# Performance work log

Hardware: AMD Instinct MI355X
Metric: run time of the kernel (lower is better)

The kernel has to match this reference:

```python
import jax, jax.numpy as jnp
import numpy as np

EPS = 1e-8
SLOPE = 0.2  # default negative_slope in VNLinearLeakyReLU
N_KNN = 4
GS_EPS = 1e-6
NOISE_SCALE = 0.1


def vn_linear(x, W):
    # x: (B, Cin, 3, ...), W: (Cout, Cin) -> (B, Cout, 3, ...)
    return jnp.einsum('oc,bc...->bo...', W, x)


def vn_linear_leaky_relu(x, Wf, Wd):
    p = vn_linear(x, Wf)
    d = vn_linear(x, Wd)
    dot = jnp.sum(p * d, axis=2, keepdims=True)
    d2 = jnp.sum(d * d, axis=2, keepdims=True)
    neg = p - (dot / (d2 + EPS)) * d
    return SLOPE * p + (1.0 - SLOPE) * jnp.where(dot >= 0, p, neg)


def vn_max_pool(x, Wd):
    # pools over the last axis using a learned direction
    d = vn_linear(x, Wd)
    dot = jnp.sum(x * d, axis=2, keepdims=True)          # (B,C,1,...,N)
    idx = jnp.argmax(dot, axis=-1)                       # (B,C,1,...)
    idx = jnp.broadcast_to(idx, x.shape[:-1])[..., None]
    return jnp.take_along_axis(x, idx, axis=-1)[..., 0]


def get_graph_feature(x, knn):
    # x: (B, C, 3, N) -> (B, 2C, 3, N, knn)
    B, C, _, N = x.shape
    xf = x.reshape(B, 3 * C, N)
    xx = jnp.sum(xf * xf, axis=1)                        # (B,N)
    inner = jnp.einsum('bdn,bdm->bnm', xf, xf)           # (B,N,N)
    neg_dist = 2.0 * inner - xx[:, :, None] - xx[:, None, :]
    _, idx = jax.lax.top_k(neg_dist, knn)                # (B,N,knn)
    pts = x.transpose(0, 3, 1, 2)                        # (B,N,C,3)
    nbrs = pts[jnp.arange(B)[:, None, None], idx]        # (B,N,knn,C,3)
    ctr = jnp.broadcast_to(pts[:, :, None], nbrs.shape)
    feat = jnp.concatenate([nbrs - ctr, ctr], axis=3)    # (B,N,knn,2C,3)
    return feat.transpose(0, 3, 4, 1, 2)


def batched_gram_schmidt_3d(M):
    # orthonormalize the columns of (B,3,3)
    def nrm(v):
        return v / (jnp.linalg.norm(v, axis=-1, keepdims=True) + EPS)
    v1, v2, v3 = M[:, :, 0], M[:, :, 1], M[:, :, 2]
    e1 = nrm(v1)
    u2 = v2 - jnp.sum(e1 * v2, -1, keepdims=True) * e1
    e2 = nrm(u2)
    u3 = v3 - jnp.sum(e1 * v3, -1, keepdims=True) * e1 - jnp.sum(e2 * v3, -1, keepdims=True) * e2
    e3 = nrm(u3)
    return jnp.stack([e1, e2, e3], axis=-1)


def setup_inputs() -> dict:
    key = jax.random.key(0)
    ks = jax.random.split(key, 10)
    b, n, d_node, d_edge, kk, dim = 4, 2048, 2, 4, 4, 32  # dim = 96 // 3
    return {
        'node_features': jax.random.normal(ks[0], (b, n, 3, d_node), jnp.float32),
        'edge_features': jax.random.normal(ks[1], (b, n, n, d_edge), jnp.float32),
        'idx': jnp.arange(b, dtype=jnp.int32),
        'k': kk,
        'W1f': jax.random.normal(ks[2], (dim, 2 * d_node), jnp.float32) * 0.3,
        'W1d': jax.random.normal(ks[3], (dim, 2 * d_node), jnp.float32) * 0.3,
        'Wp1': jax.random.normal(ks[4], (dim, dim), jnp.float32) * 0.1,
        'Wp3': jax.random.normal(ks[5], (dim, dim), jnp.float32) * 0.1,
        'Wh2': jax.random.normal(ks[6], (3, dim), jnp.float32) * 0.1,
        'z': jax.random.normal(ks[7], (b, kk, n, 3, d_node), jnp.float32) * NOISE_SCALE,
        'gs_noise': jax.random.normal(ks[8], (b, kk, 3, 3), jnp.float32),
    }


def reference(node_features, edge_features, idx, k, W1f, W1d, Wp1, Wp3, Wh2, z, gs_noise):
    b, n, _, d = node_features.shape
    # replicate k times and add invariant noise (fixed_noise=False path)
    x = jnp.broadcast_to(node_features[:, None], (b, k, n, 3, d)) + z
    x = x.reshape(b * k, n, 3, d).transpose(0, 3, 2, 1)   # (bk, d, 3, n)
    g = get_graph_feature(x, N_KNN)                       # (bk, 2d, 3, n, knn)
    h = vn_linear_leaky_relu(g, W1f, W1d)                 # (bk, dim, 3, n, knn)
    x1 = vn_max_pool(h, Wp1)                              # (bk, dim, 3, n)
    pooled = vn_max_pool(x1, Wp3)                         # (bk, dim, 3)
    pk = vn_linear(pooled, Wh2)                           # (bk, 3, 3)
    pk = pk.transpose(0, 2, 1).reshape(b, k, 3, 3)
    pk = pk + GS_EPS * gs_noise
    R = batched_gram_schmidt_3d(pk.reshape(b * k, 3, 3))
    det = jnp.linalg.det(R)                               # SO3 sign fix on column 0
    R = R.at[:, :, 0].multiply(det[:, None])
    return R.reshape(b, k, 3, 3)
```

## Files before the change

### kernel.cpp

```cpp
#include <hip/hip_runtime.h>
#include <math.h>

#define EPSF    1e-8f
#define SLOPEF  0.2f
#define GS_EPSF 1e-6f

#define NB   4
#define KZ   4
#define BKT  16
#define NPT  2048
#define DIM  32

#define COMP(v,kk) ((kk)==0?(v).x:(kk)==1?(v).y:(kk)==2?(v).z:(v).w)

__device__ __forceinline__ void fma4(float4& acc, float s, const float4& v) {
  acc.x = fmaf(s, v.x, acc.x); acc.y = fmaf(s, v.y, acc.y);
  acc.z = fmaf(s, v.z, acc.z); acc.w = fmaf(s, v.w, acc.w);
}

__global__ __launch_bounds__(256) void prep_coords(
    const float* __restrict__ node, const float* __restrict__ z,
    const float* __restrict__ Wp1, const float* __restrict__ Wp3,
    float4* __restrict__ pts, float4* __restrict__ wpk) {
  if (blockIdx.x == 0) {
    int i = threadIdx.x;
    int og = i & 7, c = i >> 3;
    wpk[i]       = make_float4(Wp1[og * 32 + c], Wp1[(og + 8) * 32 + c],
                               Wp1[(og + 16) * 32 + c], Wp1[(og + 24) * 32 + c]);
    wpk[256 + i] = make_float4(Wp3[og * 32 + c], Wp3[(og + 8) * 32 + c],
                               Wp3[(og + 16) * 32 + c], Wp3[(og + 24) * 32 + c]);
  }
  int t = blockIdx.x * 256 + threadIdx.x;
  if (t >= BKT * NPT) return;
  int bk = t >> 11, n = t & (NPT - 1);
  int b = bk >> 2, kz = bk & 3;
  const float2* np2 = (const float2*)(node + (size_t)(b * NPT + n) * 6);
  const float2* zp2 = (const float2*)(z + (size_t)((b * KZ + kz) * NPT + n) * 6);
  float ch[6];
#pragma unroll
  for (int j = 0; j < 3; ++j) {
    float2 a = np2[j], c = zp2[j];
    ch[j]     = a.x + c.x;
    ch[3 + j] = a.y + c.y;
  }
  float xx = 0.f;
#pragma unroll
  for (int h = 0; h < 6; ++h) xx = fmaf(ch[h], ch[h], xx);
  pts[(size_t)t * 2 + 0] = make_float4(ch[0], ch[1], ch[2], ch[3]);
  pts[(size_t)t * 2 + 1] = make_float4(ch[4], ch[5], xx, 0.f);
}

__device__ __forceinline__ void ins3(float s, int j,
    float& v0, float& v1, float& v2, int& i0, int& i1, int& i2) {
  bool c2 = s > v2;
  float nv2 = c2 ? s : v2; int ni2 = c2 ? j : i2;
  bool c1 = nv2 > v1;
  float u1v = c1 ? nv2 : v1, u2v = c1 ? v1 : nv2;
  int   u1i = c1 ? ni2 : i1, u2i = c1 ? i1 : ni2;
  bool c0 = u1v > v0;
  v1 = c0 ? v0 : u1v; i1 = c0 ? i0 : u1i;
  v0 = c0 ? u1v : v0; i0 = c0 ? u1i : i0;
  v2 = u2v; i2 = u2i;
}

__device__ __forceinline__ void ce(float& vx, int& ix, float& vy, int& iy) {
  float av = vx, bv = vy; int ai = ix, bi = iy;
  bool sw = (bv > av) || (bv == av && bi < ai);
  vx = sw ? bv : av; vy = sw ? av : bv;
  ix = sw ? bi : ai; iy = sw ? ai : bi;
}

__device__ __forceinline__ float score7(const float4& qa, const float4& qb,
                                        const float4& A, const float4& B) {
  float s = qa.x * A.x;
  s = fmaf(qa.y, A.y, s);
  s = fmaf(qa.z, A.z, s);
  s = fmaf(qa.w, A.w, s);
  s = fmaf(qb.x, B.x, s);
  s = fmaf(qb.y, B.y, s);
  s = fmaf(-0.5f, B.z, s);
  return s;
}

template <bool SELF>
__device__ __forceinline__ void scan128(const float4* __restrict__ pp, int j0, int q,
    const float4 qa, const float4 qb,
    float& v0, float& v1, float& v2, int& i0, int& i1, int& i2) {
  for (int t = 0; t < 128; t += 4) {
    float4 A0 = pp[2 * t + 0], B0 = pp[2 * t + 1];
    float4 A1 = pp[2 * t + 2], B1 = pp[2 * t + 3];
    float4 A2 = pp[2 * t + 4], B2 = pp[2 * t + 5];
    float4 A3 = pp[2 * t + 6], B3 = pp[2 * t + 7];
    float s0 = score7(qa, qb, A0, B0);
    float s1 = score7(qa, qb, A1, B1);
    float s2 = score7(qa, qb, A2, B2);
    float s3 = score7(qa, qb, A3, B3);
    int jb = j0 + t;
    if (SELF) {
      if (jb + 0 == q) s0 = -INFINITY;
      if (jb + 1 == q) s1 = -INFINITY;
      if (jb + 2 == q) s2 = -INFINITY;
      if (jb + 3 == q) s3 = -INFINITY;
    }
    ins3(s0, jb + 0, v0, v1, v2, i0, i1, i2);
    ins3(s1, jb + 1, v0, v1, v2, i0, i1, i2);
    ins3(s2, jb + 2, v0, v1, v2, i0, i1, i2);
    ins3(s3, jb + 3, v0, v1, v2, i0, i1, i2);
  }
}

__global__ __launch_bounds__(1024) void knn_kernel(
    const float4* __restrict__ pts, int4* __restrict__ knn4) {
  __shared__ float4 lv[16][64];
  __shared__ int4   li[16][64];
  int lane = threadIdx.x & 63;
  int w = threadIdx.x >> 6;
  int bk = blockIdx.x >> 5, qg = blockIdx.x & 31;
  int base = bk * NPT;
  int q = qg * 64 + lane;
  float4 qa = pts[(size_t)(base + q) * 2 + 0];
  float4 qb = pts[(size_t)(base + q) * 2 + 1];
  int j0 = __builtin_amdgcn_readfirstlane(w * 128);
  const float4* pp = pts + ((size_t)base + j0) * 2;
  float v0 = -INFINITY, v1 = -INFINITY, v2 = -INFINITY;
  int   i0 = 0x7fffffff, i1 = 0x7fffffff, i2 = 0x7fffffff;
  if (w == (qg >> 1)) scan128<true >(pp, j0, q, qa, qb, v0, v1, v2, i0, i1, i2);
  else                scan128<false>(pp, j0, q, qa, qb, v0, v1, v2, i0, i1, i2);
  lv[w][lane] = make_float4(v0, v1, v2, -INFINITY);
  li[w][lane] = make_int4(i0, i1, i2, 0x7fffffff);
  __syncthreads();
#pragma unroll
  for (int str = 8; str >= 1; str >>= 1) {
    if (w < str) {
      float4 av = lv[w][lane];        int4 ai = li[w][lane];
      float4 bv = lv[w + str][lane];  int4 bi = li[w + str][lane];
      float a0 = av.x, a1 = av.y, a2 = av.z, a3 = av.w;
      int   c0 = ai.x, c1 = ai.y, c2 = ai.z, c3 = ai.w;
      float s4 = bv.w, s5 = bv.z, s6 = bv.y, s7 = bv.x;
      int   t4 = bi.w, t5 = bi.z, t6 = bi.y, t7 = bi.x;
      ce(a0, c0, s4, t4); ce(a1, c1, s5, t5);
      ce(a2, c2, s6, t6); ce(a3, c3, s7, t7);
      ce(a0, c0, a2, c2); ce(a1, c1, a3, c3);
      ce(a0, c0, a1, c1); ce(a2, c2, a3, c3);
      lv[w][lane] = make_float4(a0, a1, a2, a3);
      li[w][lane] = make_int4(c0, c1, c2, c3);
    }
    __syncthreads();
  }
  if (w == 0) {
    int4 r = li[0][lane];
    knn4[base + q] = make_int4(q, r.x, r.y, r.z);
  }
}

__global__ __launch_bounds__(128) void feature_kernel(
    const float4* __restrict__ pts, const int4* __restrict__ knn4,
    const float* __restrict__ W1f, const float* __restrict__ W1d,
    const float4* __restrict__ wpk,
    float4* __restrict__ partials) {
  __shared__ float4 hlds[16][97];
  __shared__ float  dlds[16][33];
  int p = threadIdx.x >> 3;
  int og = threadIdx.x & 7;
  int bk = blockIdx.x >> 7, pb = blockIdx.x & 127;
  int n = (pb << 4) | p;
  int base = bk * NPT;
  float4 ca = pts[(size_t)(base + n) * 2 + 0], cbv = pts[(size_t)(base + n) * 2 + 1];
  float ct[6] = {ca.x, ca.y, ca.z, ca.w, cbv.x, cbv.y};
  float w1f[4][4], w1d[4][4];
#pragma unroll
  for (int m = 0; m < 4; ++m) {
    float4 wf = reinterpret_cast<const float4*>(W1f)[og + 8 * m];
    float4 wd = reinterpret_cast<const float4*>(W1d)[og + 8 * m];
    w1f[m][0] = wf.x; w1f[m][1] = wf.y; w1f[m][2] = wf.z; w1f[m][3] = wf.w;
    w1d[m][0] = wd.x; w1d[m][1] = wd.y; w1d[m][2] = wd.z; w1d[m][3] = wd.w;
  }
  int4 nb = knn4[base + n];
  int nbi[4] = {nb.x, nb.y, nb.z, nb.w};
  float h[4][4][3];
#pragma unroll
  for (int kk = 0; kk < 4; ++kk) {
    int mi = nbi[kk];
    float4 A = pts[(size_t)(base + mi) * 2 + 0], B = pts[(size_t)(base + mi) * 2 + 1];
    float nc[6] = {A.x, A.y, A.z, A.w, B.x, B.y};
    float G[4][3];
#pragma unroll
    for (int j = 0; j < 3; ++j) {
      G[0][j] = nc[j] - ct[j];
      G[1][j] = nc[3 + j] - ct[3 + j];
      G[2][j] = ct[j];
      G[3][j] = ct[3 + j];
    }
#pragma unroll
    for (int m = 0; m < 4; ++m) {
      float pvv[3], dv[3];
#pragma unroll
      for (int j = 0; j < 3; ++j) {
        float a = 0.f, dd = 0.f;
#pragma unroll
        for (int c = 0; c < 4; ++c) { a = fmaf(w1f[m][c], G[c][j], a); dd = fmaf(w1d[m][c], G[c][j], dd); }
        pvv[j] = a; dv[j] = dd;
      }
      float dot = pvv[0] * dv[0] + pvv[1] * dv[1] + pvv[2] * dv[2];
      float d2  = dv[0] * dv[0] + dv[1] * dv[1] + dv[2] * dv[2];
      float fac = dot / (d2 + EPSF);
#pragma unroll
      for (int j = 0; j < 3; ++j) {
        float negj = pvv[j] - fac * dv[j];
        float sel = (dot >= 0.f) ? pvv[j] : negj;
        h[m][kk][j] = SLOPEF * pvv[j] + (1.f - SLOPEF) * sel;
      }
    }
  }
#pragma unroll
  for (int m = 0; m < 4; ++m)
#pragma unroll
    for (int j = 0; j < 3; ++j)
      hlds[p][(og + 8 * m) * 3 + j] =
          make_float4(h[m][0][j], h[m][1][j], h[m][2][j], h[m][3][j]);
  __syncthreads();
  float4 d1j0[4], d1j1[4], d1j2[4];
#pragma unroll
  for (int m = 0; m < 4; ++m) {
    d1j0[m] = make_float4(0.f, 0.f, 0.f, 0.f);
    d1j1[m] = make_float4(0.f, 0.f, 0.f, 0.f);
    d1j2[m] = make_float4(0.f, 0.f, 0.f, 0.f);
  }
  for (int c = 0; c < 32; ++c) {
    float4 wv = wpk[c * 8 + og];
    float4 h0 = hlds[p][c * 3 + 0];
    float4 h1 = hlds[p][c * 3 + 1];
    float4 h2 = hlds[p][c * 3 + 2];
#pragma unroll
    for (int m = 0; m < 4; ++m) {
      float wm = COMP(wv, m);
      fma4(d1j0[m], wm, h0);
      fma4(d1j1[m], wm, h1);
      fma4(d1j2[m], wm, h2);
    }
  }
  float x1[4][3];
#pragma unroll
  for (int m = 0; m < 4; ++m) {
    float best = -INFINITY;
    float xa = 0.f, xb = 0.f, xc = 0.f;
#pragma unroll
    for (int kk = 0; kk < 4; ++kk) {
      float dt = h[m][kk][0] * COMP(d1j0[m], kk)
               + h[m][kk][1] * COMP(d1j1[m], kk)
               + h[m][kk][2] * COMP(d1j2[m], kk);
      if (dt > best) { best = dt; xa = h[m][kk][0]; xb = h[m][kk][1]; xc = h[m][kk][2]; }
    }
    x1[m][0] = xa; x1[m][1] = xb; x1[m][2] = xc;
  }
  __syncthreads();
#pragma unroll
  for (int m = 0; m < 4; ++m)
    hlds[p][og + 8 * m] = make_float4(x1[m][0], x1[m][1], x1[m][2], 0.f);
  __syncthreads();
  float d3[4][3] = {};
  for (int c = 0; c < 32; ++c) {
    float4 wv = wpk[256 + c * 8 + og];
    float4 xv = hlds[p][c];
#pragma unroll
    for (int m = 0; m < 4; ++m) {
      float wm = COMP(wv, m);
      d3[m][0] = fmaf(wm, xv.x, d3[m][0]);
      d3[m][1] = fmaf(wm, xv.y, d3[m][1]);
      d3[m][2] = fmaf(wm, xv.z, d3[m][2]);
    }
  }
#pragma unroll
  for (int m = 0; m < 4; ++m)
    dlds[p][og + 8 * m] = x1[m][0] * d3[m][0] + x1[m][1] * d3[m][1] + x1[m][2] * d3[m][2];
  __syncthreads();
  if (threadIdx.x < 32) {
    int o = threadIdx.x;
    float bd = -INFINITY; int wp_ = 0;
#pragma unroll
    for (int p2 = 0; p2 < 16; ++p2) {
      float dv = dlds[p2][o];
      if (dv > bd) { bd = dv; wp_ = p2; }
    }
    float4 xv = hlds[wp_][o];
    partials[(((size_t)(bk * 32 + o)) << 7) | pb] = make_float4(xv.x, xv.y, xv.z, bd);
  }
}

__global__ __launch_bounds__(256) void poolhead_kernel(
    const float4* __restrict__ partials, const float* __restrict__ Wh2,
    const float* __restrict__ gs, float* __restrict__ out) {
  __shared__ float pl[DIM][3];
  int bk = blockIdx.x;
  int o = threadIdx.x >> 3, tg = threadIdx.x & 7;
  const float4* pp = partials + (((size_t)(bk * 32 + o)) << 7);
  float best = -INFINITY; int bp = 0x7fffffff;
  for (int t = 0; t < 16; ++t) {
    int pb = t * 8 + tg;
    float v = pp[pb].w;
    if (v > best) { best = v; bp = pb; }
  }
#pragma unroll
  for (int off = 1; off < 8; off <<= 1) {
    float ov = __shfl_xor(best, off, 8);
    int   op = __shfl_xor(bp, off, 8);
    if (ov > best || (ov == best && op < bp)) { best = ov; bp = op; }
  }
  if (tg == 0) {
    float4 xv = pp[bp];
    pl[o][0] = xv.x; pl[o][1] = xv.y; pl[o][2] = xv.z;
  }
  __syncthreads();
  if (threadIdx.x == 0) {
    float M[3][3];
#pragma unroll
    for (int oo = 0; oo < 3; ++oo) {
      float a0 = 0.f, a1 = 0.f, a2 = 0.f;
      for (int c = 0; c < 32; ++c) {
        float w = Wh2[oo * 32 + c];
        a0 = fmaf(w, pl[c][0], a0);
        a1 = fmaf(w, pl[c][1], a1);
        a2 = fmaf(w, pl[c][2], a2);
      }
      M[0][oo] = a0 + GS_EPSF * gs[bk * 9 + 0 * 3 + oo];
      M[1][oo] = a1 + GS_EPSF * gs[bk * 9 + 1 * 3 + oo];
      M[2][oo] = a2 + GS_EPSF * gs[bk * 9 + 2 * 3 + oo];
    }
    float e1[3], e2[3], e3[3], u[3];
    float nn = sqrtf(M[0][0] * M[0][0] + M[1][0] * M[1][0] + M[2][0] * M[2][0]) + EPSF;
#pragma unroll
    for (int r = 0; r < 3; ++r) e1[r] = M[r][0] / nn;
    float d12 = e1[0] * M[0][1] + e1[1] * M[1][1] + e1[2] * M[2][1];
#pragma unroll
    for (int r = 0; r < 3; ++r) u[r] = M[r][1] - d12 * e1[r];
    nn = sqrtf(u[0] * u[0] + u[1] * u[1] + u[2] * u[2]) + EPSF;
#pragma unroll
    for (int r = 0; r < 3; ++r) e2[r] = u[r] / nn;
    float d13 = e1[0] * M[0][2] + e1[1] * M[1][2] + e1[2] * M[2][2];
    float d23 = e2[0] * M[0][2] + e2[1] * M[1][2] + e2[2] * M[2][2];
#pragma unroll
    for (int r = 0; r < 3; ++r) u[r] = M[r][2] - d13 * e1[r] - d23 * e2[r];
    nn = sqrtf(u[0] * u[0] + u[1] * u[1] + u[2] * u[2]) + EPSF;
#pragma unroll
    for (int r = 0; r < 3; ++r) e3[r] = u[r] / nn;
    float det = e1[0] * (e2[1] * e3[2] - e2[2] * e3[1])
              - e1[1] * (e2[0] * e3[2] - e2[2] * e3[0])
              + e1[2] * (e2[0] * e3[1] - e2[1] * e3[0]);
#pragma unroll
    for (int r = 0; r < 3; ++r) {
      out[bk * 9 + r * 3 + 0] = e1[r] * det;
      out[bk * 9 + r * 3 + 1] = e2[r];
      out[bk * 9 + r * 3 + 2] = e3[r];
    }
  }
}

extern "C" void kernel_launch(void* const* d_in, const int* in_sizes, int n_in,
                              void* d_out, int out_size, void* d_ws, size_t ws_size,
                              hipStream_t stream) {
  (void)in_sizes; (void)n_in; (void)out_size; (void)ws_size;
  const float* node = (const float*)d_in[0];
  const float* W1f = (const float*)d_in[4];
  const float* W1d = (const float*)d_in[5];
  const float* Wp1 = (const float*)d_in[6];
  const float* Wp3 = (const float*)d_in[7];
  const float* Wh2 = (const float*)d_in[8];
  const float* z   = (const float*)d_in[9];
  const float* gs  = (const float*)d_in[10];

  float4* pts      = (float4*)d_ws;
  int4*   knn4     = (int4*)(pts + (size_t)BKT * NPT * 2);
  float4* partials = (float4*)(knn4 + (size_t)BKT * NPT);
  float4* wpk      = partials + (size_t)BKT * 32 * 128;
  float*  out      = (float*)d_out;

  prep_coords    <<<BKT * NPT / 256, 256, 0, stream>>>(node, z, Wp1, Wp3, pts, wpk);
  knn_kernel     <<<BKT * 32, 1024, 0, stream>>>(pts, knn4);
  feature_kernel <<<BKT * 128, 128, 0, stream>>>(pts, knn4, W1f, W1d, wpk, partials);
  poolhead_kernel<<<BKT, 256, 0, stream>>>(partials, Wh2, gs, out);
}
```

Baseline: 82.03 us.

## Pair-interleave KNN candidate layout for packed FMA and med3 top-3 insert

prep_coords also writes a pair-interleaved copy of the point coordinates, two points per 64-byte record with each component stored as a float2. The KNN scan uses this layout to score two candidates at once with 2-wide vector FMAs, which can map to packed FP32 instructions. The top-3 insertion is rewritten branch-free using fmax and fmed3 with independent compares, which shortens the dependency chain. This costs an extra workspace buffer and extra writes in prep_coords.

```diff
diff --git a/kernel.cpp b/kernel.cpp
--- a/kernel.cpp
+++ b/kernel.cpp
@@ -13,6 +13,8 @@
 
 #define COMP(v,kk) ((kk)==0?(v).x:(kk)==1?(v).y:(kk)==2?(v).z:(v).w)
 
+typedef float f2 __attribute__((ext_vector_type(2)));
+
 __device__ __forceinline__ void fma4(float4& acc, float s, const float4& v) {
   acc.x = fmaf(s, v.x, acc.x); acc.y = fmaf(s, v.y, acc.y);
   acc.z = fmaf(s, v.z, acc.z); acc.w = fmaf(s, v.w, acc.w);
@@ -21,7 +23,8 @@
 __global__ __launch_bounds__(256) void prep_coords(
     const float* __restrict__ node, const float* __restrict__ z,
     const float* __restrict__ Wp1, const float* __restrict__ Wp3,
-    float4* __restrict__ pts, float4* __restrict__ wpk) {
+    float4* __restrict__ pts, float* __restrict__ ptsPf,
+    float4* __restrict__ wpk) {
   if (blockIdx.x == 0) {
     int i = threadIdx.x;
     int og = i & 7, c = i >> 3;
@@ -48,19 +51,22 @@
   for (int h = 0; h < 6; ++h) xx = fmaf(ch[h], ch[h], xx);
   pts[(size_t)t * 2 + 0] = make_float4(ch[0], ch[1], ch[2], ch[3]);
   pts[(size_t)t * 2 + 1] = make_float4(ch[4], ch[5], xx, 0.f);
-}
-
-__device__ __forceinline__ void ins3(float s, int j,
+  size_t pbase = (size_t)(t >> 1) * 16 + (t & 1);
+#pragma unroll
+  for (int c = 0; c < 6; ++c) ptsPf[pbase + c * 2] = ch[c];
+  ptsPf[pbase + 12] = xx;
+}
+
+__device__ __forceinline__ void ins3m(float s, int j,
     float& v0, float& v1, float& v2, int& i0, int& i1, int& i2) {
-  bool c2 = s > v2;
-  float nv2 = c2 ? s : v2; int ni2 = c2 ? j : i2;
-  bool c1 = nv2 > v1;
-  float u1v = c1 ? nv2 : v1, u2v = c1 ? v1 : nv2;
-  int   u1i = c1 ? ni2 : i1, u2i = c1 ? i1 : ni2;
-  bool c0 = u1v > v0;
-  v1 = c0 ? v0 : u1v; i1 = c0 ? i0 : u1i;
-  v0 = c0 ? u1v : v0; i0 = c0 ? u1i : i0;
-  v2 = u2v; i2 = u2i;
+  bool c0 = s > v0, c1 = s > v1, c2 = s > v2;
+  float nv0 = fmaxf(v0, s);
+  float nv1 = __builtin_amdgcn_fmed3f(v0, v1, s);
+  float nv2 = __builtin_amdgcn_fmed3f(v1, v2, s);
+  i2 = c1 ? i1 : (c2 ? j : i2);
+  i1 = c0 ? i0 : (c1 ? j : i1);
+  i0 = c0 ? j : i0;
+  v0 = nv0; v1 = nv1; v2 = nv2;
 }
 
 __device__ __forceinline__ void ce(float& vx, int& ix, float& vy, int& iy) {
@@ -70,47 +76,56 @@
   ix = sw ? bi : ai; iy = sw ? ai : bi;
 }
 
-__device__ __forceinline__ float score7(const float4& qa, const float4& qb,
-                                        const float4& A, const float4& B) {
-  float s = qa.x * A.x;
-  s = fmaf(qa.y, A.y, s);
-  s = fmaf(qa.z, A.z, s);
-  s = fmaf(qa.w, A.w, s);
-  s = fmaf(qb.x, B.x, s);
-  s = fmaf(qb.y, B.y, s);
-  s = fmaf(-0.5f, B.z, s);
-  return s;
-}
-
 template <bool SELF>
-__device__ __forceinline__ void scan128(const float4* __restrict__ pp, int j0, int q,
-    const float4 qa, const float4 qb,
+__device__ __forceinline__ void scan128P(const float4* __restrict__ pp4,
+    int j0, int q, const float4 qa, const float4 qb,
     float& v0, float& v1, float& v2, int& i0, int& i1, int& i2) {
-  for (int t = 0; t < 128; t += 4) {
-    float4 A0 = pp[2 * t + 0], B0 = pp[2 * t + 1];
-    float4 A1 = pp[2 * t + 2], B1 = pp[2 * t + 3];
-    float4 A2 = pp[2 * t + 4], B2 = pp[2 * t + 5];
-    float4 A3 = pp[2 * t + 6], B3 = pp[2 * t + 7];
-    float s0 = score7(qa, qb, A0, B0);
-    float s1 = score7(qa, qb, A1, B1);
-    float s2 = score7(qa, qb, A2, B2);
-    float s3 = score7(qa, qb, A3, B3);
-    int jb = j0 + t;
+  f2 qx = {qa.x, qa.x}, qy = {qa.y, qa.y}, qz = {qa.z, qa.z}, qw = {qa.w, qa.w};
+  f2 qu = {qb.x, qb.x}, qv = {qb.y, qb.y}, mh = {-0.5f, -0.5f};
+  const f2* pp2 = (const f2*)pp4;
+  for (int pr = 0; pr < 64; pr += 2) {
+    float4 L0a = pp4[pr * 4 + 0], L1a = pp4[pr * 4 + 1], L2a = pp4[pr * 4 + 2];
+    f2 Xa = pp2[pr * 8 + 6];
+    float4 L0b = pp4[pr * 4 + 4], L1b = pp4[pr * 4 + 5], L2b = pp4[pr * 4 + 6];
+    f2 Xb = pp2[pr * 8 + 14];
+    f2 ax = {L0a.x, L0a.y}, ay = {L0a.z, L0a.w};
+    f2 az = {L1a.x, L1a.y}, aw = {L1a.z, L1a.w};
+    f2 au = {L2a.x, L2a.y}, av = {L2a.z, L2a.w};
+    f2 sa = qx * ax;
+    sa = __builtin_elementwise_fma(qy, ay, sa);
+    sa = __builtin_elementwise_fma(qz, az, sa);
+    sa = __builtin_elementwise_fma(qw, aw, sa);
+    sa = __builtin_elementwise_fma(qu, au, sa);
+    sa = __builtin_elementwise_fma(qv, av, sa);
+    sa = __builtin_elementwise_fma(mh, Xa, sa);
+    f2 bx = {L0b.x, L0b.y}, by = {L0b.z, L0b.w};
+    f2 bz = {L1b.x, L1b.y}, bw = {L1b.z, L1b.w};
+    f2 bu = {L2b.x, L2b.y}, bv = {L2b.z, L2b.w};
+    f2 sb = qx * bx;
+    sb = __builtin_elementwise_fma(qy, by, sb);
+    sb = __builtin_elementwise_fma(qz, bz, sb);
+    sb = __builtin_elementwise_fma(qw, bw, sb);
+    sb = __builtin_elementwise_fma(qu, bu, sb);
+    sb = __builtin_elementwise_fma(qv, bv, sb);
+    sb = __builtin_elementwise_fma(mh, Xb, sb);
+    int jb = j0 + 2 * pr;
+    float s0 = sa.x, s1 = sa.y, s2 = sb.x, s3 = sb.y;
     if (SELF) {
       if (jb + 0 == q) s0 = -INFINITY;
       if (jb + 1 == q) s1 = -INFINITY;
       if (jb + 2 == q) s2 = -INFINITY;
       if (jb + 3 == q) s3 = -INFINITY;
     }
-    ins3(s0, jb + 0, v0, v1, v2, i0, i1, i2);
-    ins3(s1, jb + 1, v0, v1, v2, i0, i1, i2);
-    ins3(s2, jb + 2, v0, v1, v2, i0, i1, i2);
-    ins3(s3, jb + 3, v0, v1, v2, i0, i1, i2);
+    ins3m(s0, jb + 0, v0, v1, v2, i0, i1, i2);
+    ins3m(s1, jb + 1, v0, v1, v2, i0, i1, i2);
+    ins3m(s2, jb + 2, v0, v1, v2, i0, i1, i2);
+    ins3m(s3, jb + 3, v0, v1, v2, i0, i1, i2);
   }
 }
 
 __global__ __launch_bounds__(1024) void knn_kernel(
-    const float4* __restrict__ pts, int4* __restrict__ knn4) {
+    const float4* __restrict__ pts, const float4* __restrict__ ptsP,
+    int4* __restrict__ knn4) {
   __shared__ float4 lv[16][64];
   __shared__ int4   li[16][64];
   int lane = threadIdx.x & 63;
@@ -121,11 +136,11 @@
   float4 qa = pts[(size_t)(base + q) * 2 + 0];
   float4 qb = pts[(size_t)(base + q) * 2 + 1];
   int j0 = __builtin_amdgcn_readfirstlane(w * 128);
-  const float4* pp = pts + ((size_t)base + j0) * 2;
+  const float4* pp4 = ptsP + ((size_t)(base + j0) >> 1) * 4;
   float v0 = -INFINITY, v1 = -INFINITY, v2 = -INFINITY;
   int   i0 = 0x7fffffff, i1 = 0x7fffffff, i2 = 0x7fffffff;
-  if (w == (qg >> 1)) scan128<true >(pp, j0, q, qa, qb, v0, v1, v2, i0, i1, i2);
-  else                scan128<false>(pp, j0, q, qa, qb, v0, v1, v2, i0, i1, i2);
+  if (w == (qg >> 1)) scan128P<true >(pp4, j0, q, qa, qb, v0, v1, v2, i0, i1, i2);
+  else                scan128P<false>(pp4, j0, q, qa, qb, v0, v1, v2, i0, i1, i2);
   lv[w][lane] = make_float4(v0, v1, v2, -INFINITY);
   li[w][lane] = make_int4(i0, i1, i2, 0x7fffffff);
   __syncthreads();
@@ -372,10 +387,12 @@
   int4*   knn4     = (int4*)(pts + (size_t)BKT * NPT * 2);
   float4* partials = (float4*)(knn4 + (size_t)BKT * NPT);
   float4* wpk      = partials + (size_t)BKT * 32 * 128;
+  float4* ptsP     = wpk + 512;
   float*  out      = (float*)d_out;
 
-  prep_coords    <<<BKT * NPT / 256, 256, 0, stream>>>(node, z, Wp1, Wp3, pts, wpk);
-  knn_kernel     <<<BKT * 32, 1024, 0, stream>>>(pts, knn4);
+  prep_coords    <<<BKT * NPT / 256, 256, 0, stream>>>(node, z, Wp1, Wp3, pts,
+                                                       (float*)ptsP, wpk);
+  knn_kernel     <<<BKT * 32, 1024, 0, stream>>>(pts, ptsP, knn4);
   feature_kernel <<<BKT * 128, 128, 0, stream>>>(pts, knn4, W1f, W1d, wpk, partials);
   poolhead_kernel<<<BKT, 256, 0, stream>>>(partials, Wh2, gs, out);
 }
```

After: 80.13 us. 1.02x faster.
